# Optimization experiments

Measured on AMD Instinct MI355X. Metric: run time of the kernel, lower is better.

Reference implementation:

```python
import jax, jax.numpy as jnp
import numpy as np

N_NODES = 100000
N_EDGES = 1600000
D_FEAT = 128
N_CLASSES = 16


def setup_inputs() -> dict:
    key = jax.random.key(0)
    ks = jax.random.split(key, 7)
    return {
        "x": jax.random.normal(ks[0], (N_NODES, D_FEAT), dtype=jnp.float32),
        "edge_row": jax.random.randint(ks[1], (N_EDGES,), 0, N_NODES),
        "edge_col": jax.random.randint(ks[2], (N_EDGES,), 0, N_NODES),
        "edge_val": jax.random.uniform(ks[3], (N_EDGES,), dtype=jnp.float32),
        "w1": jax.random.normal(ks[4], (D_FEAT, D_FEAT), dtype=jnp.float32) * 0.05,
        "w2": jax.random.normal(ks[5], (D_FEAT, D_FEAT), dtype=jnp.float32) * 0.05,
        "classifier": jax.random.normal(ks[6], (D_FEAT, N_CLASSES), dtype=jnp.float32) * 0.05,
    }


def reference(x, edge_row, edge_col, edge_val, w1, w2, classifier):
    n = x.shape[0]

    def spmm(h):
        # Adj.dot(h): gather source node features, scale by edge weight, scatter-add to rows
        msgs = edge_val[:, None] * h[edge_col]          # [E, D]
        return jax.ops.segment_sum(msgs, edge_row, num_segments=n)  # [N, D]

    h = x
    for w in (w1, w2):
        h = jax.nn.relu(spmm(h) @ w)
    logits = h @ classifier                              # [N, C]
    # x[x>0]=1; x[x<=0]=0  -> hard binary threshold
    return jnp.where(logits > 0, jnp.float32(1.0), jnp.float32(0.0))
```

## Files before the change

kernel.cpp:

```cpp
#include <hip/hip_runtime.h>
#include <climits>

#define D 128

typedef float f32x4 __attribute__((ext_vector_type(4)));
typedef int   i32x2 __attribute__((ext_vector_type(2)));

__global__ __launch_bounds__(256) void hist_rank_kernel(const int* __restrict__ erow,
                                                        int* __restrict__ deg,
                                                        int* __restrict__ rank, int nE) {
    int e = blockIdx.x * 256 + threadIdx.x;
    if (e < nE) rank[e] = atomicAdd(&deg[erow[e]], 1);
}

__global__ __launch_bounds__(256) void scan1_kernel(const int* __restrict__ deg,
                                                    int* __restrict__ rowptr,
                                                    int* __restrict__ blocksums, int n) {
    __shared__ int sd[256];
    const int t = threadIdx.x;
    const int idx = blockIdx.x * 1024 + t * 4;
    int4 v = make_int4(0, 0, 0, 0);
    if (idx + 3 < n) v = *(const int4*)&deg[idx];
    else {
        if (idx + 0 < n) v.x = deg[idx + 0];
        if (idx + 1 < n) v.y = deg[idx + 1];
        if (idx + 2 < n) v.z = deg[idx + 2];
        if (idx + 3 < n) v.w = deg[idx + 3];
    }
    const int s = v.x + v.y + v.z + v.w;
    sd[t] = s;
    __syncthreads();
    for (int off = 1; off < 256; off <<= 1) {
        int tv = (t >= off) ? sd[t - off] : 0;
        __syncthreads();
        sd[t] += tv;
        __syncthreads();
    }
    const int excl = sd[t] - s;
    int a = excl + v.x, b = a + v.y, c = b + v.z, d = c + v.w;
    if (idx + 0 < n) rowptr[idx + 1] = a;
    if (idx + 1 < n) rowptr[idx + 2] = b;
    if (idx + 2 < n) rowptr[idx + 3] = c;
    if (idx + 3 < n) rowptr[idx + 4] = d;
    if (t == 255) blocksums[blockIdx.x] = sd[255];
}

__global__ __launch_bounds__(256) void scan2_kernel(int* __restrict__ blocksums, int nb) {
    __shared__ int sd[256];
    const int t = threadIdx.x;
    const int v = (t < nb) ? blocksums[t] : 0;
    sd[t] = v;
    __syncthreads();
    for (int off = 1; off < 256; off <<= 1) {
        int tv = (t >= off) ? sd[t - off] : 0;
        __syncthreads();
        sd[t] += tv;
        __syncthreads();
    }
    if (t < nb) blocksums[t] = sd[t] - v;
}

__global__ __launch_bounds__(256) void scan3_kernel(int* __restrict__ rowptr,
                                                    const int* __restrict__ blocksums, int n) {
    int i = blockIdx.x * 256 + threadIdx.x;
    if (i < n) rowptr[i + 1] += blocksums[i >> 10];
    if (i == 0) rowptr[0] = 0;
}

__global__ __launch_bounds__(256) void place_kernel(const int* __restrict__ erow,
                                                    const int* __restrict__ rank,
                                                    const int* __restrict__ ecol,
                                                    const float* __restrict__ ev,
                                                    const int* __restrict__ rowptr,
                                                    i32x2* __restrict__ cv, int nE) {
    int e = blockIdx.x * 256 + threadIdx.x;
    if (e >= nE) return;
    int pos = rowptr[erow[e]] + rank[e];
    i32x2 rec;
    rec.x = ecol[e];
    rec.y = __float_as_int(ev[e]);
    cv[pos] = rec;
}

__global__ __launch_bounds__(256) void sortrow_wave_kernel(const int* __restrict__ rowptr,
                                                           i32x2* __restrict__ cv, int n) {
    int row = blockIdx.x * 4 + (threadIdx.x >> 6);
    if (row >= n) return;
    const int lane = threadIdx.x & 63;
    const int s = rowptr[row], e = rowptr[row + 1];
    const int deg = e - s;
    if (deg <= 1) return;
    if (deg <= 64) {
        unsigned long long key = ~0ull;
        i32x2 rec;
        rec.x = 0; rec.y = 0;
        if (lane < deg) {
            rec = cv[s + lane];
            key = ((unsigned long long)(unsigned)rec.x << 32) | (unsigned)rec.y;
        }
        int rank = 0;
        for (int i = 0; i < deg; ++i) {
            unsigned long long ki = __shfl(key, i);
            rank += (ki < key || (ki == key && i < lane)) ? 1 : 0;
        }
        if (lane < deg) cv[s + rank] = rec;
    } else if (lane == 0) {
        for (int i = s + 1; i < e; ++i) {
            i32x2 r_ = cv[i];
            unsigned long long k_ = ((unsigned long long)(unsigned)r_.x << 32) | (unsigned)r_.y;
            int j = i - 1;
            while (j >= s) {
                i32x2 rj = cv[j];
                unsigned long long kj = ((unsigned long long)(unsigned)rj.x << 32) | (unsigned)rj.y;
                if (kj <= k_) break;
                cv[j + 1] = rj;
                --j;
            }
            cv[j + 1] = r_;
        }
    }
}

template <bool CLASSIFY>
__global__ __launch_bounds__(256) void spmm_gemm_kernel(
        const float* __restrict__ h, const int* __restrict__ rowptr,
        const i32x2* __restrict__ cv, const float* __restrict__ W,
        const float* __restrict__ Cls, float* __restrict__ O, int n) {
    const int wid = (blockIdx.x * 256 + threadIdx.x) >> 6;
    const int lane = threadIdx.x & 63;
    const int half = lane >> 5;
    const int l = lane & 31;
    const int row0 = wid * 8;
    if (row0 >= n) return;

    const f32x4* hl = (const f32x4*)h + l;
    f32x4 rowdata[4];
#pragma unroll
    for (int i = 0; i < 4; ++i) {
        const int r = row0 + 2 * i + half;
        f32x4 acc = (f32x4)(0.f);
        if (r < n) {
            const int s = rowptr[r], e = rowptr[r + 1];
            int k = s;
            for (; k + 8 <= e; k += 8) {
                i32x2 p[8];
#pragma unroll
                for (int u = 0; u < 8; ++u) p[u] = cv[k + u];
                f32x4 hv[8];
#pragma unroll
                for (int u = 0; u < 8; ++u) hv[u] = hl[(size_t)p[u].x * 32];
#pragma unroll
                for (int u = 0; u < 8; ++u) acc += __int_as_float(p[u].y) * hv[u];
            }
            for (; k < e; ++k) {
                i32x2 p = cv[k];
                acc += __int_as_float(p.y) * hl[(size_t)p.x * 32];
            }
        }
        rowdata[i] = acc;
    }

    const int c0 = l * 4;
    const int sbase = half << 5;
    f32x4 oacc[4];
#pragma unroll
    for (int i = 0; i < 4; ++i) oacc[i] = (f32x4)(0.f);

    for (int k4 = 0; k4 < D / 4; ++k4) {
        const int srcl = sbase + k4;
#pragma unroll
        for (int kk = 0; kk < 4; ++kk) {
            const f32x4 w = *(const f32x4*)&W[(k4 * 4 + kk) * D + c0];
#pragma unroll
            for (int i = 0; i < 4; ++i) {
                float hk = __shfl(rowdata[i][kk], srcl);
                oacc[i] += hk * w;
            }
        }
    }

    if (!CLASSIFY) {
#pragma unroll
        for (int i = 0; i < 4; ++i) {
            const int r = row0 + 2 * i + half;
            if (r < n) {
                f32x4 v;
                v.x = fmaxf(oacc[i].x, 0.f); v.y = fmaxf(oacc[i].y, 0.f);
                v.z = fmaxf(oacc[i].z, 0.f); v.w = fmaxf(oacc[i].w, 0.f);
                *(f32x4*)&O[(size_t)r * D + c0] = v;
            }
        }
    } else {
#pragma unroll
        for (int i = 0; i < 4; ++i) {
            oacc[i].x = fmaxf(oacc[i].x, 0.f); oacc[i].y = fmaxf(oacc[i].y, 0.f);
            oacc[i].z = fmaxf(oacc[i].z, 0.f); oacc[i].w = fmaxf(oacc[i].w, 0.f);
        }
        const int j = l & 15;
        const int kh = l >> 4;
        float lg[4] = {0.f, 0.f, 0.f, 0.f};
        for (int m4 = 0; m4 < 16; ++m4) {
            const int srcl = sbase + kh * 16 + m4;
#pragma unroll
            for (int kk = 0; kk < 4; ++kk) {
                const int k = kh * 64 + m4 * 4 + kk;
                const float c = Cls[k * 16 + j];
#pragma unroll
                for (int i = 0; i < 4; ++i) {
                    float hk = __shfl(oacc[i][kk], srcl);
                    lg[i] += hk * c;
                }
            }
        }
#pragma unroll
        for (int i = 0; i < 4; ++i) lg[i] += __shfl_xor(lg[i], 16);
        if (kh == 0) {
#pragma unroll
            for (int i = 0; i < 4; ++i) {
                const int r = row0 + 2 * i + half;
                if (r < n) O[(size_t)r * 16 + j] = lg[i] > 0.f ? 1.f : 0.f;
            }
        }
    }
}

extern "C" void kernel_launch(void* const* d_in, const int* in_sizes, int n_in,
                              void* d_out, int out_size, void* d_ws, size_t ws_size,
                              hipStream_t stream) {
    const float* x    = (const float*)d_in[0];
    const int*   erow = (const int*)d_in[1];
    const int*   ecol = (const int*)d_in[2];
    const float* ev   = (const float*)d_in[3];
    const float* w1   = (const float*)d_in[4];
    const float* w2   = (const float*)d_in[5];
    const float* cls  = (const float*)d_in[6];

    const int n  = in_sizes[0] / D;
    const int nE = in_sizes[1];

    char*  ws     = (char*)d_ws;
    float* h      = (float*)ws;                 ws += (size_t)n * D * 4;
    int*   deg    = (int*)ws;                   ws += (size_t)n * 4;
    int*   rowptr = (int*)ws;                   ws += (size_t)(n + 1) * 4;
    int*   rank   = (int*)ws;                   ws += (size_t)nE * 4;
    i32x2* cv     = (i32x2*)ws;                 ws += (size_t)nE * 8;
    int*   bsums  = (int*)ws;                   ws += 256 * 4;

    const int nb = (n + 1023) / 1024;

    dim3 blk(256);
    dim3 egrid((nE + 255) / 256);
    dim3 ngrid((n + 255) / 256);
    dim3 wgrid((n + 3) / 4);
    dim3 sgrid((n + 31) / 32);

    (void)hipMemsetAsync(deg, 0, (size_t)n * 4, stream);
    hist_rank_kernel<<<egrid, blk, 0, stream>>>(erow, deg, rank, nE);
    scan1_kernel<<<nb, blk, 0, stream>>>(deg, rowptr, bsums, n);
    scan2_kernel<<<1, blk, 0, stream>>>(bsums, nb);
    scan3_kernel<<<ngrid, blk, 0, stream>>>(rowptr, bsums, n);
    place_kernel<<<egrid, blk, 0, stream>>>(erow, rank, ecol, ev, rowptr, cv, nE);
    sortrow_wave_kernel<<<wgrid, blk, 0, stream>>>(rowptr, cv, n);

    spmm_gemm_kernel<false><<<sgrid, blk, 0, stream>>>(x, rowptr, cv, w1, nullptr, h, n);

    spmm_gemm_kernel<true><<<sgrid, blk, 0, stream>>>(h, rowptr, cv, w2, cls,
                                                      (float*)d_out, n);
}
```

Before: 474.4 us.

## Pad CSR rows to multiples of eight and halve rows per wave

Each row's degree is rounded up to a multiple of 8 in the scan, and the padding slots are filled with zero-weight records pointing at column 0. The SpMM loop then runs only in full 8-wide unrolled chunks with no scalar tail. Separately, each wave now handles 4 rows instead of 8, doubling the grid for more parallelism while reusing each W load across fewer rows. Padding adds extra edges (about 3.5 per row on average) that gather row 0, plus more CSR storage.

```diff
diff --git a/kernel.cpp b/kernel.cpp
--- a/kernel.cpp
+++ b/kernel.cpp
@@ -27,6 +27,8 @@
         if (idx + 2 < n) v.z = deg[idx + 2];
         if (idx + 3 < n) v.w = deg[idx + 3];
     }
+    v.x = (v.x + 7) & ~7; v.y = (v.y + 7) & ~7;
+    v.z = (v.z + 7) & ~7; v.w = (v.w + 7) & ~7;
     const int s = v.x + v.y + v.z + v.w;
     sd[t] = s;
     __syncthreads();
@@ -83,29 +85,31 @@
 }
 
 __global__ __launch_bounds__(256) void sortrow_wave_kernel(const int* __restrict__ rowptr,
+                                                           const int* __restrict__ deg,
                                                            i32x2* __restrict__ cv, int n) {
     int row = blockIdx.x * 4 + (threadIdx.x >> 6);
     if (row >= n) return;
     const int lane = threadIdx.x & 63;
-    const int s = rowptr[row], e = rowptr[row + 1];
-    const int deg = e - s;
-    if (deg <= 1) return;
-    if (deg <= 64) {
+    const int s = rowptr[row], pe = rowptr[row + 1];
+    const int dg = deg[row];
+    const int npad = pe - s - dg;
+    i32x2 zero; zero.x = 0; zero.y = 0;
+    if (dg <= 64) {
         unsigned long long key = ~0ull;
-        i32x2 rec;
-        rec.x = 0; rec.y = 0;
-        if (lane < deg) {
+        i32x2 rec = zero;
+        if (lane < dg) {
             rec = cv[s + lane];
             key = ((unsigned long long)(unsigned)rec.x << 32) | (unsigned)rec.y;
         }
         int rank = 0;
-        for (int i = 0; i < deg; ++i) {
+        for (int i = 0; i < dg; ++i) {
             unsigned long long ki = __shfl(key, i);
             rank += (ki < key || (ki == key && i < lane)) ? 1 : 0;
         }
-        if (lane < deg) cv[s + rank] = rec;
+        if (lane < dg) cv[s + rank] = rec;
+        if (lane < npad) cv[s + dg + lane] = zero;
     } else if (lane == 0) {
-        for (int i = s + 1; i < e; ++i) {
+        for (int i = s + 1; i < s + dg; ++i) {
             i32x2 r_ = cv[i];
             unsigned long long k_ = ((unsigned long long)(unsigned)r_.x << 32) | (unsigned)r_.y;
             int j = i - 1;
@@ -118,6 +122,7 @@
             }
             cv[j + 1] = r_;
         }
+        for (int i = s + dg; i < pe; ++i) cv[i] = zero;
     }
 }
 
@@ -130,19 +135,18 @@
     const int lane = threadIdx.x & 63;
     const int half = lane >> 5;
     const int l = lane & 31;
-    const int row0 = wid * 8;
+    const int row0 = wid * 4;
     if (row0 >= n) return;
 
     const f32x4* hl = (const f32x4*)h + l;
-    f32x4 rowdata[4];
-#pragma unroll
-    for (int i = 0; i < 4; ++i) {
+    f32x4 rowdata[2];
+#pragma unroll
+    for (int i = 0; i < 2; ++i) {
         const int r = row0 + 2 * i + half;
         f32x4 acc = (f32x4)(0.f);
         if (r < n) {
             const int s = rowptr[r], e = rowptr[r + 1];
-            int k = s;
-            for (; k + 8 <= e; k += 8) {
+            for (int k = s; k < e; k += 8) {
                 i32x2 p[8];
 #pragma unroll
                 for (int u = 0; u < 8; ++u) p[u] = cv[k + u];
@@ -152,19 +156,15 @@
 #pragma unroll
                 for (int u = 0; u < 8; ++u) acc += __int_as_float(p[u].y) * hv[u];
             }
-            for (; k < e; ++k) {
-                i32x2 p = cv[k];
-                acc += __int_as_float(p.y) * hl[(size_t)p.x * 32];
-            }
         }
         rowdata[i] = acc;
     }
 
     const int c0 = l * 4;
     const int sbase = half << 5;
-    f32x4 oacc[4];
-#pragma unroll
-    for (int i = 0; i < 4; ++i) oacc[i] = (f32x4)(0.f);
+    f32x4 oacc[2];
+#pragma unroll
+    for (int i = 0; i < 2; ++i) oacc[i] = (f32x4)(0.f);
 
     for (int k4 = 0; k4 < D / 4; ++k4) {
         const int srcl = sbase + k4;
@@ -172,7 +172,7 @@
         for (int kk = 0; kk < 4; ++kk) {
             const f32x4 w = *(const f32x4*)&W[(k4 * 4 + kk) * D + c0];
 #pragma unroll
-            for (int i = 0; i < 4; ++i) {
+            for (int i = 0; i < 2; ++i) {
                 float hk = __shfl(rowdata[i][kk], srcl);
                 oacc[i] += hk * w;
             }
@@ -181,7 +181,7 @@
 
     if (!CLASSIFY) {
 #pragma unroll
-        for (int i = 0; i < 4; ++i) {
+        for (int i = 0; i < 2; ++i) {
             const int r = row0 + 2 * i + half;
             if (r < n) {
                 f32x4 v;
@@ -192,13 +192,13 @@
         }
     } else {
 #pragma unroll
-        for (int i = 0; i < 4; ++i) {
+        for (int i = 0; i < 2; ++i) {
             oacc[i].x = fmaxf(oacc[i].x, 0.f); oacc[i].y = fmaxf(oacc[i].y, 0.f);
             oacc[i].z = fmaxf(oacc[i].z, 0.f); oacc[i].w = fmaxf(oacc[i].w, 0.f);
         }
         const int j = l & 15;
         const int kh = l >> 4;
-        float lg[4] = {0.f, 0.f, 0.f, 0.f};
+        float lg[2] = {0.f, 0.f};
         for (int m4 = 0; m4 < 16; ++m4) {
             const int srcl = sbase + kh * 16 + m4;
 #pragma unroll
@@ -206,17 +206,17 @@
                 const int k = kh * 64 + m4 * 4 + kk;
                 const float c = Cls[k * 16 + j];
 #pragma unroll
-                for (int i = 0; i < 4; ++i) {
+                for (int i = 0; i < 2; ++i) {
                     float hk = __shfl(oacc[i][kk], srcl);
                     lg[i] += hk * c;
                 }
             }
         }
 #pragma unroll
-        for (int i = 0; i < 4; ++i) lg[i] += __shfl_xor(lg[i], 16);
+        for (int i = 0; i < 2; ++i) lg[i] += __shfl_xor(lg[i], 16);
         if (kh == 0) {
 #pragma unroll
-            for (int i = 0; i < 4; ++i) {
+            for (int i = 0; i < 2; ++i) {
                 const int r = row0 + 2 * i + half;
                 if (r < n) O[(size_t)r * 16 + j] = lg[i] > 0.f ? 1.f : 0.f;
             }
@@ -243,7 +243,7 @@
     int*   deg    = (int*)ws;                   ws += (size_t)n * 4;
     int*   rowptr = (int*)ws;                   ws += (size_t)(n + 1) * 4;
     int*   rank   = (int*)ws;                   ws += (size_t)nE * 4;
-    i32x2* cv     = (i32x2*)ws;                 ws += (size_t)nE * 8;
+    i32x2* cv     = (i32x2*)ws;                 ws += ((size_t)nE + 8 * (size_t)n) * 8;
     int*   bsums  = (int*)ws;                   ws += 256 * 4;
 
     const int nb = (n + 1023) / 1024;
@@ -252,7 +252,7 @@
     dim3 egrid((nE + 255) / 256);
     dim3 ngrid((n + 255) / 256);
     dim3 wgrid((n + 3) / 4);
-    dim3 sgrid((n + 31) / 32);
+    dim3 sgrid((n + 15) / 16);
 
     (void)hipMemsetAsync(deg, 0, (size_t)n * 4, stream);
     hist_rank_kernel<<<egrid, blk, 0, stream>>>(erow, deg, rank, nE);
@@ -260,7 +260,7 @@
     scan2_kernel<<<1, blk, 0, stream>>>(bsums, nb);
     scan3_kernel<<<ngrid, blk, 0, stream>>>(rowptr, bsums, n);
     place_kernel<<<egrid, blk, 0, stream>>>(erow, rank, ecol, ev, rowptr, cv, nE);
-    sortrow_wave_kernel<<<wgrid, blk, 0, stream>>>(rowptr, cv, n);
+    sortrow_wave_kernel<<<wgrid, blk, 0, stream>>>(rowptr, deg, cv, n);
 
     spmm_gemm_kernel<false><<<sgrid, blk, 0, stream>>>(x, rowptr, cv, w1, nullptr, h, n);
 
```

Result: no change. 473.0 us (-0.3%).
